# Kernel tuning notes

Measured on AMD Instinct MI355X. Metric: run time of the kernel, lower is better.

Reference implementation:

```python
import jax, jax.numpy as jnp
import numpy as np

EMBED_DIM = 1024
N_HEADS = 16
HEAD_DIM = EMBED_DIM // N_HEADS
EPS = 1e-6


def setup_inputs() -> dict:
    key = jax.random.key(0)
    k_x, k_wqkv, k_bqkv, k_wo, k_bo = jax.random.split(key, 5)
    B, T, C = 2, 2048, EMBED_DIM
    s = 1.0 / np.sqrt(C)
    return {
        "x": jax.random.normal(k_x, (B, T, C), dtype=jnp.float32),
        "w_qkv": jax.random.normal(k_wqkv, (C, 3 * C), dtype=jnp.float32) * s,
        "b_qkv": jax.random.normal(k_bqkv, (3 * C,), dtype=jnp.float32) * s,
        "w_out": jax.random.normal(k_wo, (C, C), dtype=jnp.float32) * s,
        "b_out": jax.random.normal(k_bo, (C,), dtype=jnp.float32) * s,
    }


def reference(x, w_qkv, b_qkv, w_out, b_out):
    B, T, C = x.shape
    H, D = N_HEADS, HEAD_DIM
    qkv = x @ w_qkv + b_qkv                       # [B,T,3C]
    q, k, v = jnp.split(qkv, 3, axis=-1)
    # [B,H,T,D]
    q = q.reshape(B, T, H, D).transpose(0, 2, 1, 3)
    k = k.reshape(B, T, H, D).transpose(0, 2, 1, 3)
    v = v.reshape(B, T, H, D).transpose(0, 2, 1, 3)
    dot = jnp.einsum("bhqd,bhkd->bhqk", q, k)     # [B,H,T,T]
    q_sq = jnp.sum(q * q, axis=-1)[..., :, None]  # [B,H,T,1]
    k_sq = jnp.sum(k * k, axis=-1)[..., None, :]  # [B,H,1,T]
    scores = (dot * dot) / (q_sq + k_sq - 2.0 * dot + EPS)
    causal = jnp.tril(jnp.ones((T, T), dtype=bool))
    scores = jnp.where(causal, scores, -jnp.inf)
    attn = jax.nn.softmax(scores, axis=-1)
    out = jnp.einsum("bhqk,bhkd->bhqd", attn, v)  # [B,H,T,D]
    out = out.transpose(0, 2, 1, 3).reshape(B, T, C)
    return out @ w_out + b_out
```

## Files before the change

### kernel.cpp

```cpp
#include <hip/hip_runtime.h>
#include <stdint.h>


#define TSEQ 2048
#define BATCH 2

typedef _Float16 f16x8 __attribute__((ext_vector_type(8)));
typedef __fp16 fp16x2 __attribute__((ext_vector_type(2)));
typedef float f32x4 __attribute__((ext_vector_type(4)));
typedef unsigned int u32x2 __attribute__((ext_vector_type(2)));

#define MFMA16(a, b, c) __builtin_amdgcn_mfma_f32_16x16x32_f16(a, b, c, 0, 0, 0)

__device__ __forceinline__ unsigned short f2h(float f) {
  union { _Float16 h; unsigned short u; } v;
  v.h = (_Float16)f;
  return v.u;
}
__device__ __forceinline__ float h2f(unsigned short u) {
  union { unsigned short u; _Float16 h; } v;
  v.u = u;
  return (float)v.h;
}
__device__ __forceinline__ unsigned int pack2h(float lo, float hi) {
  return (unsigned int)f2h(lo) | ((unsigned int)f2h(hi) << 16);
}
__device__ __forceinline__ float sumsq_u32(unsigned int u) {
  float lo = h2f(u & 0xffffu);
  float hi = h2f(u >> 16);
  return lo * lo + hi * hi;
}
__device__ __forceinline__ void async_ld16(const void* g, const void* l) {
  __builtin_amdgcn_global_load_lds((const __attribute__((address_space(1))) void*)g,
                                   (__attribute__((address_space(3))) void*)l,
                                   16, 0, 0);
}
__device__ __forceinline__ unsigned int pk_f16(float lo, float hi) {
  union { fp16x2 h; unsigned int u; } c;
  c.h = __builtin_amdgcn_cvt_pkrtz(lo, hi);
  return c.u;
}

__global__ __launch_bounds__(256) void cvt_x(const float* __restrict__ src,
                                             unsigned short* __restrict__ dst) {
  const int i = (blockIdx.x * 256 + threadIdx.x) * 8;
  const float4 a = *(const float4*)(src + i);
  const float4 b = *(const float4*)(src + i + 4);
  uint4 o;
  o.x = pack2h(a.x, a.y); o.y = pack2h(a.z, a.w);
  o.z = pack2h(b.x, b.y); o.w = pack2h(b.z, b.w);
  *(uint4*)(dst + i) = o;
}

__global__ __launch_bounds__(256) void transpose_w(const float* __restrict__ src,
                                                   unsigned short* __restrict__ dst,
                                                   int K, int N) {
  __shared__ unsigned short tile[32][33];
  const int tx = threadIdx.x, ty = threadIdx.y;
  const int nb = blockIdx.x * 32, kb = blockIdx.y * 32;
#pragma unroll
  for (int i = 0; i < 4; i++)
    tile[ty + 8 * i][tx] = f2h(src[(size_t)(kb + ty + 8 * i) * N + nb + tx]);
  __syncthreads();
#pragma unroll
  for (int i = 0; i < 4; i++)
    dst[(size_t)(nb + ty + 8 * i) * K + kb + tx] = tile[tx][ty + 8 * i];
}

template <int TN, bool OUT_F32>
__global__ __launch_bounds__(256) void gemm_bt(const unsigned short* __restrict__ A,
                                               const unsigned short* __restrict__ Bt,
                                               const float* __restrict__ bias,
                                               void* __restrict__ Cp,
                                               int N, int K) {
  __shared__ __attribute__((aligned(16))) unsigned short Atile[128 * 32];
  __shared__ __attribute__((aligned(16))) unsigned short Btile[TN * 32];
  constexpr int NJ = TN / 32;
  const int tid = threadIdx.x;
  const int w = tid >> 6, lane = tid & 63;
  const int quad = lane >> 4, l15 = lane & 15;
  const int m0 = blockIdx.y * 128, n0 = blockIdx.x * TN;
  const int wr = w >> 1, wc = w & 1;
  const int nwc = wc * (TN / 2);
  f32x4 acc[4][NJ] = {};
  for (int kt = 0; kt < K; kt += 32) {
    __syncthreads();
#pragma unroll
    for (int it = 0; it < 2; it++) {
      const int c = it * 256 + tid;
      async_ld16(A + (size_t)(m0 + (c >> 2)) * K + kt + (c & 3) * 8,
                 &Atile[(size_t)(it * 256 + w * 64) * 8]);
    }
#pragma unroll
    for (int it = 0; it < TN / 64; it++) {
      const int c = it * 256 + tid;
      async_ld16(Bt + (size_t)(n0 + (c >> 2)) * K + kt + (c & 3) * 8,
                 &Btile[(size_t)(it * 256 + w * 64) * 8]);
    }
    __syncthreads();
    f16x8 af[4], bfr[NJ];
#pragma unroll
    for (int i = 0; i < 4; i++)
      af[i] = *(const f16x8*)&Atile[(wr * 64 + i * 16 + l15) * 32 + quad * 8];
#pragma unroll
    for (int j = 0; j < NJ; j++)
      bfr[j] = *(const f16x8*)&Btile[(nwc + j * 16 + l15) * 32 + quad * 8];
#pragma unroll
    for (int i = 0; i < 4; i++)
#pragma unroll
      for (int j = 0; j < NJ; j++)
        acc[i][j] = MFMA16(af[i], bfr[j], acc[i][j]);
  }
#pragma unroll
  for (int j = 0; j < NJ; j++) {
    const int n = n0 + nwc + j * 16 + l15;
    const float bv = bias[n];
#pragma unroll
    for (int i = 0; i < 4; i++) {
      const int mb = m0 + wr * 64 + i * 16 + quad * 4;
#pragma unroll
      for (int r = 0; r < 4; r++) {
        if constexpr (OUT_F32)
          ((float*)Cp)[(size_t)(mb + r) * N + n] = acc[i][j][r] + bv;
        else
          ((unsigned short*)Cp)[(size_t)(mb + r) * N + n] = f2h(acc[i][j][r] + bv);
      }
    }
  }
}

__global__ __launch_bounds__(256, 4) void yat_attn(const unsigned short* __restrict__ qkv,
                                                   unsigned short* __restrict__ outp) {
  __shared__ __attribute__((aligned(16))) unsigned short Kp[2][64 * 72];
  __shared__ __attribute__((aligned(16))) unsigned short Vt[2][64 * 72];
  __shared__ float qsq[64], ksq[2][64];
  const int tid = threadIdx.x;
  const int w = tid >> 6, lane = tid & 63;
  const int quad = lane >> 4, l15 = lane & 15;
  const int bh = blockIdx.x, b = bh >> 4, h = bh & 15;
  const int y = blockIdx.y;
  const int qt = (y < 8) ? 31 - y : (y < 16) ? y - 8 : (y < 24) ? 39 - y : y - 16;
  const unsigned short* base = qkv + (size_t)b * TSEQ * 3072 + h * 64;
  const int t = tid >> 2, dc = (tid & 3) * 16;
  const int d0 = tid & 31, tg8 = tid >> 5;

  uint4 kreg0, kreg1;
  unsigned int vreg[8];
  {
    const unsigned short* gk = base + 1024 + (size_t)t * 3072 + dc;
    kreg0 = *(const uint4*)gk;
    kreg1 = *(const uint4*)(gk + 8);
    const unsigned short* gv = base + 2048 + (size_t)(tg8 * 8) * 3072 + 2 * d0;
#pragma unroll
    for (int s = 0; s < 8; s++)
      vreg[s] = *(const unsigned int*)(gv + (size_t)s * 3072);
  }
  {
    const unsigned short* g = base + (size_t)(qt * 64 + t) * 3072 + dc;
    uint4 v0 = *(const uint4*)g;
    uint4 v1 = *(const uint4*)(g + 8);
    *(uint4*)&Kp[1][t * 72 + dc] = v0;
    *(uint4*)&Kp[1][t * 72 + dc + 8] = v1;
    float s = sumsq_u32(v0.x) + sumsq_u32(v0.y) + sumsq_u32(v0.z) + sumsq_u32(v0.w) +
              sumsq_u32(v1.x) + sumsq_u32(v1.y) + sumsq_u32(v1.z) + sumsq_u32(v1.w);
    s += __shfl_xor(s, 1);
    s += __shfl_xor(s, 2);
    if ((tid & 3) == 0) qsq[t] = s;
  }
  auto commit = [&](int buf) {
    *(uint4*)&Kp[buf][t * 72 + dc] = kreg0;
    *(uint4*)&Kp[buf][t * 72 + dc + 8] = kreg1;
    float s = sumsq_u32(kreg0.x) + sumsq_u32(kreg0.y) + sumsq_u32(kreg0.z) +
              sumsq_u32(kreg0.w) + sumsq_u32(kreg1.x) + sumsq_u32(kreg1.y) +
              sumsq_u32(kreg1.z) + sumsq_u32(kreg1.w);
    s += __shfl_xor(s, 1);
    s += __shfl_xor(s, 2);
    if ((tid & 3) == 0) ksq[buf][t] = s;
    uint4 LO, HI;
    LO.x = (vreg[0] & 0xffffu) | (vreg[1] << 16);
    LO.y = (vreg[2] & 0xffffu) | (vreg[3] << 16);
    LO.z = (vreg[4] & 0xffffu) | (vreg[5] << 16);
    LO.w = (vreg[6] & 0xffffu) | (vreg[7] << 16);
    HI.x = (vreg[0] >> 16) | (vreg[1] & 0xffff0000u);
    HI.y = (vreg[2] >> 16) | (vreg[3] & 0xffff0000u);
    HI.z = (vreg[4] >> 16) | (vreg[5] & 0xffff0000u);
    HI.w = (vreg[6] >> 16) | (vreg[7] & 0xffff0000u);
    *(uint4*)&Vt[buf][(2 * d0) * 72 + tg8 * 8] = LO;
    *(uint4*)&Vt[buf][(2 * d0 + 1) * 72 + tg8 * 8] = HI;
  };
  commit(0);
  if (qt >= 1) {
    const unsigned short* gk = base + 1024 + (size_t)(64 + t) * 3072 + dc;
    kreg0 = *(const uint4*)gk;
    kreg1 = *(const uint4*)(gk + 8);
    const unsigned short* gv = base + 2048 + (size_t)(64 + tg8 * 8) * 3072 + 2 * d0;
#pragma unroll
    for (int s = 0; s < 8; s++)
      vreg[s] = *(const unsigned int*)(gv + (size_t)s * 3072);
  }
  __syncthreads();
  const f16x8 aq0 = *(const f16x8*)&Kp[1][(w * 16 + l15) * 72 + quad * 8];
  const f16x8 aq1 = *(const f16x8*)&Kp[1][(w * 16 + l15) * 72 + 32 + quad * 8];
  const f16x8 onesf = {(_Float16)1.f, (_Float16)1.f, (_Float16)1.f, (_Float16)1.f,
                       (_Float16)1.f, (_Float16)1.f, (_Float16)1.f, (_Float16)1.f};
  const int ql = w * 16 + l15;
  const float qsq_eps = qsq[ql] + 1e-6f;
  __syncthreads();

  f32x4 accO[4] = {};
  float m_run = 0.f;
  float l_acc = 0.f;

  for (int kt = 0; kt <= qt; kt++) {
    const int cur = kt & 1;
    f32x4 accS[4] = {};
#pragma unroll
    for (int nt = 0; nt < 4; nt++) {
      const f16x8 bk0 = *(const f16x8*)&Kp[cur][(nt * 16 + l15) * 72 + quad * 8];
      const f16x8 bk1 = *(const f16x8*)&Kp[cur][(nt * 16 + l15) * 72 + 32 + quad * 8];
      accS[nt] = MFMA16(bk0, aq0, accS[nt]);
      accS[nt] = MFMA16(bk1, aq1, accS[nt]);
    }
    float pv[4][4];
#pragma unroll
    for (int nt = 0; nt < 4; nt++) {
      const f32x4 k4 = *(const f32x4*)&ksq[cur][nt * 16 + quad * 4];
#pragma unroll
      for (int r = 0; r < 4; r++) {
        const float d = accS[nt][r];
        const float den = __builtin_fmaf(-2.f, d, k4[r] + qsq_eps);
        pv[nt][r] = d * d * __builtin_amdgcn_rcpf(den);
      }
    }
    if (kt == qt) {
#pragma unroll
      for (int nt = 0; nt < 4; nt++)
#pragma unroll
        for (int r = 0; r < 4; r++)
          if (nt * 16 + quad * 4 + r > ql) pv[nt][r] = -1e30f;
    }
    float tm = fmaxf(fmaxf(fmaxf(pv[0][0], pv[0][1]), fmaxf(pv[0][2], pv[0][3])),
                     fmaxf(fmaxf(pv[1][0], pv[1][1]), fmaxf(pv[1][2], pv[1][3])));
    tm = fmaxf(tm, fmaxf(fmaxf(fmaxf(pv[2][0], pv[2][1]), fmaxf(pv[2][2], pv[2][3])),
                         fmaxf(fmaxf(pv[3][0], pv[3][1]), fmaxf(pv[3][2], pv[3][3]))));
    tm = fmaxf(tm, __shfl_xor(tm, 16));
    tm = fmaxf(tm, __shfl_xor(tm, 32));
    const float mn = fmaxf(m_run, tm);
    const float alpha = __expf(m_run - mn);
    m_run = mn;
    unsigned int pa[4], pb[4];
#pragma unroll
    for (int nt = 0; nt < 4; nt++) {
      pa[nt] = pk_f16(__expf(pv[nt][0] - mn), __expf(pv[nt][1] - mn));
      pb[nt] = pk_f16(__expf(pv[nt][2] - mn), __expf(pv[nt][3] - mn));
    }
    if (kt < qt) commit(cur ^ 1);
    if (kt + 2 <= qt) {
      const unsigned short* gk = base + 1024 + (size_t)((kt + 2) * 64 + t) * 3072 + dc;
      kreg0 = *(const uint4*)gk;
      kreg1 = *(const uint4*)(gk + 8);
      const unsigned short* gv =
          base + 2048 + (size_t)((kt + 2) * 64 + tg8 * 8) * 3072 + 2 * d0;
#pragma unroll
      for (int s = 0; s < 8; s++)
        vreg[s] = *(const unsigned int*)(gv + (size_t)s * 3072);
    }
    union { f16x8 v; unsigned int u[4]; } bp0, bp1;
    {
      u32x2 s0 = __builtin_amdgcn_permlane32_swap(pa[0], pa[1], false, false);
      u32x2 s1 = __builtin_amdgcn_permlane16_swap(s0.x, s0.y, false, false);
      bp0.u[0] = s1.x; bp0.u[2] = s1.y;
      s0 = __builtin_amdgcn_permlane32_swap(pb[0], pb[1], false, false);
      s1 = __builtin_amdgcn_permlane16_swap(s0.x, s0.y, false, false);
      bp0.u[1] = s1.x; bp0.u[3] = s1.y;
      s0 = __builtin_amdgcn_permlane32_swap(pa[2], pa[3], false, false);
      s1 = __builtin_amdgcn_permlane16_swap(s0.x, s0.y, false, false);
      bp1.u[0] = s1.x; bp1.u[2] = s1.y;
      s0 = __builtin_amdgcn_permlane32_swap(pb[2], pb[3], false, false);
      s1 = __builtin_amdgcn_permlane16_swap(s0.x, s0.y, false, false);
      bp1.u[1] = s1.x; bp1.u[3] = s1.y;
    }
#pragma unroll
    for (int i = 0; i < 4; i++) {
      accO[i][0] *= alpha; accO[i][1] *= alpha;
      accO[i][2] *= alpha; accO[i][3] *= alpha;
    }
    f32x4 accL = {};
    accL = MFMA16(onesf, bp0.v, accL);
    accL = MFMA16(onesf, bp1.v, accL);
#pragma unroll
    for (int i = 0; i < 4; i++) {
      const f16x8 av0 = *(const f16x8*)&Vt[cur][(i * 16 + l15) * 72 + quad * 8];
      const f16x8 av1 = *(const f16x8*)&Vt[cur][(i * 16 + l15) * 72 + 32 + quad * 8];
      accO[i] = MFMA16(av0, bp0.v, accO[i]);
      accO[i] = MFMA16(av1, bp1.v, accO[i]);
    }
    l_acc = l_acc * alpha + accL[0];
    __syncthreads();
  }

  const float linv = 1.0f / l_acc;
#pragma unroll
  for (int i = 0; i < 4; i++)
#pragma unroll
    for (int r = 0; r < 4; r++)
      Kp[0][(w * 16 + l15) * 72 + i * 16 + quad * 4 + r] = f2h(accO[i][r] * linv);
  __syncthreads();
  {
    uint4 o0 = *(const uint4*)&Kp[0][t * 72 + dc];
    uint4 o1 = *(const uint4*)&Kp[0][t * 72 + dc + 8];
    unsigned short* g = outp + (size_t)(b * TSEQ + qt * 64 + t) * 1024 + h * 64 + dc;
    *(uint4*)g = o0;
    *(uint4*)(g + 8) = o1;
  }
}

extern "C" void kernel_launch(void* const* d_in, const int* in_sizes, int n_in,
                              void* d_out, int out_size, void* d_ws, size_t ws_size,
                              hipStream_t stream) {
  (void)in_sizes; (void)n_in; (void)out_size; (void)ws_size;
  const float* x     = (const float*)d_in[0];
  const float* w_qkv = (const float*)d_in[1];
  const float* b_qkv = (const float*)d_in[2];
  const float* w_out = (const float*)d_in[3];
  const float* b_out = (const float*)d_in[4];
  float* out = (float*)d_out;

  unsigned short* wqkvT  = (unsigned short*)d_ws;
  unsigned short* woT    = wqkvT + (size_t)3072 * 1024;
  unsigned short* qkvws  = woT + (size_t)1024 * 1024;
  unsigned short* xh     = qkvws + (size_t)4096 * 3072;
  unsigned short* attnws = xh;

  cvt_x<<<dim3(4096 * 1024 / (256 * 8)), 256, 0, stream>>>(x, xh);
  transpose_w<<<dim3(3072 / 32, 1024 / 32), dim3(32, 8), 0, stream>>>(w_qkv, wqkvT, 1024, 3072);
  transpose_w<<<dim3(1024 / 32, 1024 / 32), dim3(32, 8), 0, stream>>>(w_out, woT, 1024, 1024);
  gemm_bt<128, false><<<dim3(3072 / 128, 4096 / 128), 256, 0, stream>>>(xh, wqkvT, b_qkv, qkvws, 3072, 1024);
  yat_attn<<<dim3(BATCH * 16, 32), 256, 0, stream>>>(qkvws, attnws);
  gemm_bt<64, true><<<dim3(1024 / 64, 4096 / 128), 256, 0, stream>>>(attnws, woT, b_out, out, 1024, 1024);
}
```

Baseline: 194.8 us.

## Process two 64-row query tiles per attention block to reuse K/V tiles

Each attention workgroup now handles 128 query rows (two 64-row halves) instead of 64, so every K/V tile loaded into shared memory feeds twice as many MFMAs. The grid halves to 16 blocks per head and the query-tile ordering is remapped for load balance, with a separate final iteration handling the diagonal tile for the upper half. This cuts global K/V traffic and per-tile sync overhead, but raises register pressure (two accumulator sets) and reduces the number of blocks available to fill the GPU.

```diff
diff --git a/kernel.cpp b/kernel.cpp
--- a/kernel.cpp
+++ b/kernel.cpp
@@ -133,13 +133,15 @@
                                                    unsigned short* __restrict__ outp) {
   __shared__ __attribute__((aligned(16))) unsigned short Kp[2][64 * 72];
   __shared__ __attribute__((aligned(16))) unsigned short Vt[2][64 * 72];
-  __shared__ float qsq[64], ksq[2][64];
+  __shared__ float qsq[128], ksq[2][64];
   const int tid = threadIdx.x;
   const int w = tid >> 6, lane = tid & 63;
   const int quad = lane >> 4, l15 = lane & 15;
   const int bh = blockIdx.x, b = bh >> 4, h = bh & 15;
-  const int y = blockIdx.y;
-  const int qt = (y < 8) ? 31 - y : (y < 16) ? y - 8 : (y < 24) ? 39 - y : y - 16;
+  const int y = blockIdx.y, i7 = y & 7;
+  const int yp = (y < 8) ? (15 - i7 - 2 * ((i7 + 1) >> 1)) : (14 - i7 - 2 * (i7 >> 1));
+  const int NT = 2 * yp + 2;
+  const int q0 = yp * 128;
   const unsigned short* base = qkv + (size_t)b * TSEQ * 3072 + h * 64;
   const int t = tid >> 2, dc = (tid & 3) * 16;
   const int d0 = tid & 31, tg8 = tid >> 5;
@@ -156,9 +158,9 @@
       vreg[s] = *(const unsigned int*)(gv + (size_t)s * 3072);
   }
   {
-    const unsigned short* g = base + (size_t)(qt * 64 + t) * 3072 + dc;
-    uint4 v0 = *(const uint4*)g;
-    uint4 v1 = *(const uint4*)(g + 8);
+    const unsigned short* gL = base + (size_t)(q0 + t) * 3072 + dc;
+    uint4 v0 = *(const uint4*)gL;
+    uint4 v1 = *(const uint4*)(gL + 8);
     *(uint4*)&Kp[1][t * 72 + dc] = v0;
     *(uint4*)&Kp[1][t * 72 + dc + 8] = v1;
     float s = sumsq_u32(v0.x) + sumsq_u32(v0.y) + sumsq_u32(v0.z) + sumsq_u32(v0.w) +
@@ -166,6 +168,16 @@
     s += __shfl_xor(s, 1);
     s += __shfl_xor(s, 2);
     if ((tid & 3) == 0) qsq[t] = s;
+    const unsigned short* gH = base + (size_t)(q0 + 64 + t) * 3072 + dc;
+    v0 = *(const uint4*)gH;
+    v1 = *(const uint4*)(gH + 8);
+    *(uint4*)&Vt[1][t * 72 + dc] = v0;
+    *(uint4*)&Vt[1][t * 72 + dc + 8] = v1;
+    s = sumsq_u32(v0.x) + sumsq_u32(v0.y) + sumsq_u32(v0.z) + sumsq_u32(v0.w) +
+        sumsq_u32(v1.x) + sumsq_u32(v1.y) + sumsq_u32(v1.z) + sumsq_u32(v1.w);
+    s += __shfl_xor(s, 1);
+    s += __shfl_xor(s, 2);
+    if ((tid & 3) == 0) qsq[64 + t] = s;
   }
   auto commit = [&](int buf) {
     *(uint4*)&Kp[buf][t * 72 + dc] = kreg0;
@@ -189,7 +201,7 @@
     *(uint4*)&Vt[buf][(2 * d0 + 1) * 72 + tg8 * 8] = HI;
   };
   commit(0);
-  if (qt >= 1) {
+  {
     const unsigned short* gk = base + 1024 + (size_t)(64 + t) * 3072 + dc;
     kreg0 = *(const uint4*)gk;
     kreg1 = *(const uint4*)(gk + 8);
@@ -199,46 +211,23 @@
       vreg[s] = *(const unsigned int*)(gv + (size_t)s * 3072);
   }
   __syncthreads();
-  const f16x8 aq0 = *(const f16x8*)&Kp[1][(w * 16 + l15) * 72 + quad * 8];
-  const f16x8 aq1 = *(const f16x8*)&Kp[1][(w * 16 + l15) * 72 + 32 + quad * 8];
+  const f16x8 aq0L = *(const f16x8*)&Kp[1][(w * 16 + l15) * 72 + quad * 8];
+  const f16x8 aq1L = *(const f16x8*)&Kp[1][(w * 16 + l15) * 72 + 32 + quad * 8];
+  const f16x8 aq0H = *(const f16x8*)&Vt[1][(w * 16 + l15) * 72 + quad * 8];
+  const f16x8 aq1H = *(const f16x8*)&Vt[1][(w * 16 + l15) * 72 + 32 + quad * 8];
   const f16x8 onesf = {(_Float16)1.f, (_Float16)1.f, (_Float16)1.f, (_Float16)1.f,
                        (_Float16)1.f, (_Float16)1.f, (_Float16)1.f, (_Float16)1.f};
-  const int ql = w * 16 + l15;
-  const float qsq_eps = qsq[ql] + 1e-6f;
+  const int wl = w * 16 + l15;
+  const float qeL = qsq[wl] + 1e-6f;
+  const float qeH = qsq[64 + wl] + 1e-6f;
   __syncthreads();
 
-  f32x4 accO[4] = {};
-  float m_run = 0.f;
-  float l_acc = 0.f;
-
-  for (int kt = 0; kt <= qt; kt++) {
-    const int cur = kt & 1;
-    f32x4 accS[4] = {};
-#pragma unroll
-    for (int nt = 0; nt < 4; nt++) {
-      const f16x8 bk0 = *(const f16x8*)&Kp[cur][(nt * 16 + l15) * 72 + quad * 8];
-      const f16x8 bk1 = *(const f16x8*)&Kp[cur][(nt * 16 + l15) * 72 + 32 + quad * 8];
-      accS[nt] = MFMA16(bk0, aq0, accS[nt]);
-      accS[nt] = MFMA16(bk1, aq1, accS[nt]);
-    }
-    float pv[4][4];
-#pragma unroll
-    for (int nt = 0; nt < 4; nt++) {
-      const f32x4 k4 = *(const f32x4*)&ksq[cur][nt * 16 + quad * 4];
-#pragma unroll
-      for (int r = 0; r < 4; r++) {
-        const float d = accS[nt][r];
-        const float den = __builtin_fmaf(-2.f, d, k4[r] + qsq_eps);
-        pv[nt][r] = d * d * __builtin_amdgcn_rcpf(den);
-      }
-    }
-    if (kt == qt) {
-#pragma unroll
-      for (int nt = 0; nt < 4; nt++)
-#pragma unroll
-        for (int r = 0; r < 4; r++)
-          if (nt * 16 + quad * 4 + r > ql) pv[nt][r] = -1e30f;
-    }
+  f32x4 accOL[4] = {}, accOH[4] = {};
+  float mL = 0.f, mH = 0.f;
+  float lL = 0.f, lH = 0.f;
+
+  auto soft_pack = [&](float pv[4][4], float& m_run, float& alpha,
+                       f16x8& bp0v, f16x8& bp1v) {
     float tm = fmaxf(fmaxf(fmaxf(pv[0][0], pv[0][1]), fmaxf(pv[0][2], pv[0][3])),
                      fmaxf(fmaxf(pv[1][0], pv[1][1]), fmaxf(pv[1][2], pv[1][3])));
     tm = fmaxf(tm, fmaxf(fmaxf(fmaxf(pv[2][0], pv[2][1]), fmaxf(pv[2][2], pv[2][3])),
@@ -246,7 +235,7 @@
     tm = fmaxf(tm, __shfl_xor(tm, 16));
     tm = fmaxf(tm, __shfl_xor(tm, 32));
     const float mn = fmaxf(m_run, tm);
-    const float alpha = __expf(m_run - mn);
+    alpha = __expf(m_run - mn);
     m_run = mn;
     unsigned int pa[4], pb[4];
 #pragma unroll
@@ -254,8 +243,61 @@
       pa[nt] = pk_f16(__expf(pv[nt][0] - mn), __expf(pv[nt][1] - mn));
       pb[nt] = pk_f16(__expf(pv[nt][2] - mn), __expf(pv[nt][3] - mn));
     }
-    if (kt < qt) commit(cur ^ 1);
-    if (kt + 2 <= qt) {
+    union { f16x8 v; unsigned int u[4]; } bp0, bp1;
+    u32x2 s0 = __builtin_amdgcn_permlane32_swap(pa[0], pa[1], false, false);
+    u32x2 s1 = __builtin_amdgcn_permlane16_swap(s0.x, s0.y, false, false);
+    bp0.u[0] = s1.x; bp0.u[2] = s1.y;
+    s0 = __builtin_amdgcn_permlane32_swap(pb[0], pb[1], false, false);
+    s1 = __builtin_amdgcn_permlane16_swap(s0.x, s0.y, false, false);
+    bp0.u[1] = s1.x; bp0.u[3] = s1.y;
+    s0 = __builtin_amdgcn_permlane32_swap(pa[2], pa[3], false, false);
+    s1 = __builtin_amdgcn_permlane16_swap(s0.x, s0.y, false, false);
+    bp1.u[0] = s1.x; bp1.u[2] = s1.y;
+    s0 = __builtin_amdgcn_permlane32_swap(pb[2], pb[3], false, false);
+    s1 = __builtin_amdgcn_permlane16_swap(s0.x, s0.y, false, false);
+    bp1.u[1] = s1.x; bp1.u[3] = s1.y;
+    bp0v = bp0.v; bp1v = bp1.v;
+  };
+
+  for (int kt = 0; kt <= NT - 2; kt++) {
+    const int cur = kt & 1;
+    f32x4 aSL[4] = {}, aSH[4] = {};
+#pragma unroll
+    for (int nt = 0; nt < 4; nt++) {
+      const f16x8 bk0 = *(const f16x8*)&Kp[cur][(nt * 16 + l15) * 72 + quad * 8];
+      const f16x8 bk1 = *(const f16x8*)&Kp[cur][(nt * 16 + l15) * 72 + 32 + quad * 8];
+      aSL[nt] = MFMA16(bk0, aq0L, aSL[nt]);
+      aSL[nt] = MFMA16(bk1, aq1L, aSL[nt]);
+      aSH[nt] = MFMA16(bk0, aq0H, aSH[nt]);
+      aSH[nt] = MFMA16(bk1, aq1H, aSH[nt]);
+    }
+    float pvL[4][4], pvH[4][4];
+#pragma unroll
+    for (int nt = 0; nt < 4; nt++) {
+      const f32x4 k4 = *(const f32x4*)&ksq[cur][nt * 16 + quad * 4];
+#pragma unroll
+      for (int r = 0; r < 4; r++) {
+        float d = aSL[nt][r];
+        float den = __builtin_fmaf(-2.f, d, k4[r] + qeL);
+        pvL[nt][r] = d * d * __builtin_amdgcn_rcpf(den);
+        d = aSH[nt][r];
+        den = __builtin_fmaf(-2.f, d, k4[r] + qeH);
+        pvH[nt][r] = d * d * __builtin_amdgcn_rcpf(den);
+      }
+    }
+    if (kt == NT - 2) {
+#pragma unroll
+      for (int nt = 0; nt < 4; nt++)
+#pragma unroll
+        for (int r = 0; r < 4; r++)
+          if (nt * 16 + quad * 4 + r > wl) pvL[nt][r] = -1e30f;
+    }
+    float alphaL, alphaH;
+    f16x8 bpL0, bpL1, bpH0, bpH1;
+    soft_pack(pvL, mL, alphaL, bpL0, bpL1);
+    soft_pack(pvH, mH, alphaH, bpH0, bpH1);
+    commit(cur ^ 1);
+    if (kt + 2 <= NT - 1) {
       const unsigned short* gk = base + 1024 + (size_t)((kt + 2) * 64 + t) * 3072 + dc;
       kreg0 = *(const uint4*)gk;
       kreg1 = *(const uint4*)(gk + 8);
@@ -265,51 +307,94 @@
       for (int s = 0; s < 8; s++)
         vreg[s] = *(const unsigned int*)(gv + (size_t)s * 3072);
     }
-    union { f16x8 v; unsigned int u[4]; } bp0, bp1;
-    {
-      u32x2 s0 = __builtin_amdgcn_permlane32_swap(pa[0], pa[1], false, false);
-      u32x2 s1 = __builtin_amdgcn_permlane16_swap(s0.x, s0.y, false, false);
-      bp0.u[0] = s1.x; bp0.u[2] = s1.y;
-      s0 = __builtin_amdgcn_permlane32_swap(pb[0], pb[1], false, false);
-      s1 = __builtin_amdgcn_permlane16_swap(s0.x, s0.y, false, false);
-      bp0.u[1] = s1.x; bp0.u[3] = s1.y;
-      s0 = __builtin_amdgcn_permlane32_swap(pa[2], pa[3], false, false);
-      s1 = __builtin_amdgcn_permlane16_swap(s0.x, s0.y, false, false);
-      bp1.u[0] = s1.x; bp1.u[2] = s1.y;
-      s0 = __builtin_amdgcn_permlane32_swap(pb[2], pb[3], false, false);
-      s1 = __builtin_amdgcn_permlane16_swap(s0.x, s0.y, false, false);
-      bp1.u[1] = s1.x; bp1.u[3] = s1.y;
-    }
 #pragma unroll
     for (int i = 0; i < 4; i++) {
-      accO[i][0] *= alpha; accO[i][1] *= alpha;
-      accO[i][2] *= alpha; accO[i][3] *= alpha;
-    }
-    f32x4 accL = {};
-    accL = MFMA16(onesf, bp0.v, accL);
-    accL = MFMA16(onesf, bp1.v, accL);
+      accOL[i][0] *= alphaL; accOL[i][1] *= alphaL;
+      accOL[i][2] *= alphaL; accOL[i][3] *= alphaL;
+      accOH[i][0] *= alphaH; accOH[i][1] *= alphaH;
+      accOH[i][2] *= alphaH; accOH[i][3] *= alphaH;
+    }
+    f32x4 aLL = {}, aLH = {};
+    aLL = MFMA16(onesf, bpL0, aLL);
+    aLL = MFMA16(onesf, bpL1, aLL);
+    aLH = MFMA16(onesf, bpH0, aLH);
+    aLH = MFMA16(onesf, bpH1, aLH);
 #pragma unroll
     for (int i = 0; i < 4; i++) {
       const f16x8 av0 = *(const f16x8*)&Vt[cur][(i * 16 + l15) * 72 + quad * 8];
       const f16x8 av1 = *(const f16x8*)&Vt[cur][(i * 16 + l15) * 72 + 32 + quad * 8];
-      accO[i] = MFMA16(av0, bp0.v, accO[i]);
-      accO[i] = MFMA16(av1, bp1.v, accO[i]);
-    }
-    l_acc = l_acc * alpha + accL[0];
+      accOL[i] = MFMA16(av0, bpL0, accOL[i]);
+      accOL[i] = MFMA16(av1, bpL1, accOL[i]);
+      accOH[i] = MFMA16(av0, bpH0, accOH[i]);
+      accOH[i] = MFMA16(av1, bpH1, accOH[i]);
+    }
+    lL = lL * alphaL + aLL[0];
+    lH = lH * alphaH + aLH[0];
     __syncthreads();
   }
-
-  const float linv = 1.0f / l_acc;
+  {
+    const int cur = (NT - 1) & 1;
+    f32x4 aSH[4] = {};
+#pragma unroll
+    for (int nt = 0; nt < 4; nt++) {
+      const f16x8 bk0 = *(const f16x8*)&Kp[cur][(nt * 16 + l15) * 72 + quad * 8];
+      const f16x8 bk1 = *(const f16x8*)&Kp[cur][(nt * 16 + l15) * 72 + 32 + quad * 8];
+      aSH[nt] = MFMA16(bk0, aq0H, aSH[nt]);
+      aSH[nt] = MFMA16(bk1, aq1H, aSH[nt]);
+    }
+    float pvH[4][4];
+#pragma unroll
+    for (int nt = 0; nt < 4; nt++) {
+      const f32x4 k4 = *(const f32x4*)&ksq[cur][nt * 16 + quad * 4];
+#pragma unroll
+      for (int r = 0; r < 4; r++) {
+        const float d = aSH[nt][r];
+        const float den = __builtin_fmaf(-2.f, d, k4[r] + qeH);
+        float sc = d * d * __builtin_amdgcn_rcpf(den);
+        if (nt * 16 + quad * 4 + r > wl) sc = -1e30f;
+        pvH[nt][r] = sc;
+      }
+    }
+    float alphaH;
+    f16x8 bpH0, bpH1;
+    soft_pack(pvH, mH, alphaH, bpH0, bpH1);
+#pragma unroll
+    for (int i = 0; i < 4; i++) {
+      accOH[i][0] *= alphaH; accOH[i][1] *= alphaH;
+      accOH[i][2] *= alphaH; accOH[i][3] *= alphaH;
+    }
+    f32x4 aLH = {};
+    aLH = MFMA16(onesf, bpH0, aLH);
+    aLH = MFMA16(onesf, bpH1, aLH);
+#pragma unroll
+    for (int i = 0; i < 4; i++) {
+      const f16x8 av0 = *(const f16x8*)&Vt[cur][(i * 16 + l15) * 72 + quad * 8];
+      const f16x8 av1 = *(const f16x8*)&Vt[cur][(i * 16 + l15) * 72 + 32 + quad * 8];
+      accOH[i] = MFMA16(av0, bpH0, accOH[i]);
+      accOH[i] = MFMA16(av1, bpH1, accOH[i]);
+    }
+    lH = lH * alphaH + aLH[0];
+  }
+
+  __syncthreads();
+  const float liL = 1.0f / lL, liH = 1.0f / lH;
 #pragma unroll
   for (int i = 0; i < 4; i++)
 #pragma unroll
-    for (int r = 0; r < 4; r++)
-      Kp[0][(w * 16 + l15) * 72 + i * 16 + quad * 4 + r] = f2h(accO[i][r] * linv);
+    for (int r = 0; r < 4; r++) {
+      Kp[0][(w * 16 + l15) * 72 + i * 16 + quad * 4 + r] = f2h(accOL[i][r] * liL);
+      Kp[1][(w * 16 + l15) * 72 + i * 16 + quad * 4 + r] = f2h(accOH[i][r] * liH);
+    }
   __syncthreads();
   {
     uint4 o0 = *(const uint4*)&Kp[0][t * 72 + dc];
     uint4 o1 = *(const uint4*)&Kp[0][t * 72 + dc + 8];
-    unsigned short* g = outp + (size_t)(b * TSEQ + qt * 64 + t) * 1024 + h * 64 + dc;
+    unsigned short* g = outp + (size_t)(b * TSEQ + q0 + t) * 1024 + h * 64 + dc;
+    *(uint4*)g = o0;
+    *(uint4*)(g + 8) = o1;
+    o0 = *(const uint4*)&Kp[1][t * 72 + dc];
+    o1 = *(const uint4*)&Kp[1][t * 72 + dc + 8];
+    g = outp + (size_t)(b * TSEQ + q0 + 64 + t) * 1024 + h * 64 + dc;
     *(uint4*)g = o0;
     *(uint4*)(g + 8) = o1;
   }
@@ -336,6 +421,6 @@
   transpose_w<<<dim3(3072 / 32, 1024 / 32), dim3(32, 8), 0, stream>>>(w_qkv, wqkvT, 1024, 3072);
   transpose_w<<<dim3(1024 / 32, 1024 / 32), dim3(32, 8), 0, stream>>>(w_out, woT, 1024, 1024);
   gemm_bt<128, false><<<dim3(3072 / 128, 4096 / 128), 256, 0, stream>>>(xh, wqkvT, b_qkv, qkvws, 3072, 1024);
-  yat_attn<<<dim3(BATCH * 16, 32), 256, 0, stream>>>(qkvws, attnws);
+  yat_attn<<<dim3(BATCH * 16, 16), 256, 0, stream>>>(qkvws, attnws);
   gemm_bt<64, true><<<dim3(1024 / 64, 4096 / 128), 256, 0, stream>>>(attnws, woT, b_out, out, 1024, 1024);
 }
```

New measurement: 322.0 us. 65.3% more time.
